# Kernel tuning notes

Measured on AMD Instinct MI355X. Metric: run time of the kernel, lower is better.

Reference implementation:

```python
import jax, jax.numpy as jnp
import numpy as np

V = 100000
E = 1600000
IN_CH = 128
HEADS = 4
OUT_CH = 16
NEG_SLOPE = 0.2


def setup_inputs() -> dict:
    key = jax.random.key(0)
    k1, k2, k3, k4, k5 = jax.random.split(key, 5)
    x = jax.random.normal(k1, (V, IN_CH), dtype=jnp.float32)
    edge_index = jax.random.randint(k2, (2, E), 0, V, dtype=jnp.int32)
    # Xavier-ish scaled params
    W = jax.random.normal(k3, (IN_CH, HEADS * OUT_CH), dtype=jnp.float32) / np.sqrt(IN_CH)
    a_src = jax.random.normal(k4, (HEADS, OUT_CH), dtype=jnp.float32) / np.sqrt(OUT_CH)
    a_dst = jax.random.normal(k5, (HEADS, OUT_CH), dtype=jnp.float32) / np.sqrt(OUT_CH)
    return {"x": x, "edge_index": edge_index, "W": W, "a_src": a_src, "a_dst": a_dst}


def reference(x, edge_index, W, a_src, a_dst):
    v = x.shape[0]
    h, cout = a_src.shape
    z = (x @ W).reshape(v, h, cout)                      # [V,H,C]
    src, dst = edge_index[0], edge_index[1]
    # per-node attention logits, then gather at edges (same math as gather-then-dot)
    e_src = jnp.einsum("vhc,hc->vh", z, a_src)           # [V,H]
    e_dst = jnp.einsum("vhc,hc->vh", z, a_dst)           # [V,H]
    e = jax.nn.leaky_relu(e_src[src] + e_dst[dst], NEG_SLOPE)  # [E,H]
    # scatter softmax over dst per head
    m = jax.ops.segment_max(e, dst, num_segments=v)      # [V,H]
    # nodes with no incoming edges get -inf max; edges never reference them
    exp_e = jnp.exp(e - m[dst])                          # [E,H]
    denom = jax.ops.segment_sum(exp_e, dst, num_segments=v)  # [V,H]
    alpha = exp_e / (denom[dst] + 1e-9)                  # [E,H]
    # scatter aggregation of weighted source features
    agg = jax.ops.segment_sum(z[src] * alpha[:, :, None], dst, num_segments=v)  # [V,H,C]
    out = jax.nn.elu(agg)
    return out.reshape(v, h * cout)
```

## Files before the change

kernel.cpp:

```cpp
#include <hip/hip_runtime.h>
#include <hip/hip_bf16.h>
#include <cstdint>

#define NV 100000
#define NE 1600000
#define KIN 128
#define NH 4
#define NC 16
#define NF 64
#define NBKT 1563
#define BCAP 1216
#define EPW 16
#define BINWG 391
#define GEMMWG 1563
#define XSTR 136

typedef __attribute__((ext_vector_type(8))) short bf16x8;
typedef __attribute__((ext_vector_type(4))) float f32x4;

__device__ __forceinline__ short f2bf(float f) {
    unsigned u = __float_as_uint(f);
    return (short)((u + 0x7FFFu + ((u >> 16) & 1u)) >> 16);
}

__device__ __forceinline__ unsigned enc11(float w) {
    unsigned t = (__float_as_uint(w) + 0x10000u) >> 17;
    t = min(max(t, 7168u), 9215u);
    return t - 7168u;
}

__global__ __launch_bounds__(256) void k_prep(
    const float* __restrict__ W, const float* __restrict__ a_src,
    const float* __restrict__ a_dst, short* __restrict__ wfrag,
    int* __restrict__ gcur)
{
    const int g = blockIdx.x * 256 + threadIdx.x;
    if (g < NBKT) gcur[g] = 0;
    if (g < 1280) {
        const int lane = g & 63;
        const int ctks = g >> 6;
        const int ct = ctks >> 2, ks = ctks & 3;
        const int n = lane & 15, quad = lane >> 4;
        short* dst = wfrag + (size_t)g * 8;
#pragma unroll
        for (int j = 0; j < 8; ++j) {
            const int k = ks * 32 + quad * 8 + j;
            float v = 0.f;
            if (ct < 4) {
                v = W[k * NF + ct * 16 + n];
            } else if (n < 8) {
                const int h = n & 3;
                const float* __restrict__ a =
                    (n < 4) ? (a_src + h * 16) : (a_dst + h * 16);
                for (int c = 0; c < 16; ++c)
                    v += W[k * NF + h * 16 + c] * a[c];
            }
            dst[j] = f2bf(v);
        }
    }
}

__global__ __launch_bounds__(256) void k_front(
    const float* __restrict__ x, const short* __restrict__ wfrag,
    __hip_bfloat16* __restrict__ z, float* __restrict__ esrc,
    float* __restrict__ edst,
    const int* __restrict__ ei, int* __restrict__ gcur,
    unsigned* __restrict__ barr)
{
    __shared__ union SM {
        struct { int hist[NBKT]; int base[NBKT]; } bin;
        short xs[64 * XSTR];
    } sm;

    if (blockIdx.x % 5 == 0) {
        int* hist = sm.bin.hist;
        int* base = sm.bin.base;
        const int t = threadIdx.x;
        const int e0 = (blockIdx.x / 5) * (256 * EPW);

        for (int i = t; i < NBKT; i += 256) hist[i] = 0;
        __syncthreads();

        unsigned pk[EPW];
        short bk[EPW];
#pragma unroll
        for (int i = 0; i < EPW; ++i) {
            const int e = e0 + i * 256 + t;
            if (e < NE) {
                const int s = ei[e];
                const int d = ei[NE + e];
                const int bkt = d >> 6;
                bk[i] = (short)bkt;
                pk[i] = ((unsigned)(d & 63) << 17) | (unsigned)s;
                atomicAdd(&hist[bkt], 1);
            } else {
                bk[i] = -1;
            }
        }
        __syncthreads();
        for (int i = t; i < NBKT; i += 256) {
            const int c = hist[i];
            base[i] = c ? atomicAdd(&gcur[i], c) : 0;
            hist[i] = 0;
        }
        __syncthreads();
#pragma unroll
        for (int i = 0; i < EPW; ++i) {
            if (bk[i] >= 0) {
                const int bkt = bk[i];
                const int pos = base[bkt] + atomicAdd(&hist[bkt], 1);
                if (pos < BCAP)
                    barr[(size_t)bkt * BCAP + pos] = pk[i];
            }
        }
    } else {
        short* xs = sm.xs;
        const int t = threadIdx.x;
        const int bb = blockIdx.x - blockIdx.x / 5 - 1;
        const float4* __restrict__ x4 = (const float4*)x;

#pragma unroll
        for (int i = 0; i < 8; ++i) {
            const int li = i * 256 + t;
            const int idx = bb * 2048 + li;
            float4 v = make_float4(0.f, 0.f, 0.f, 0.f);
            if (idx < NV * (KIN / 4)) v = x4[idx];
            const unsigned lo = (unsigned)(unsigned short)f2bf(v.x)
                              | ((unsigned)(unsigned short)f2bf(v.y) << 16);
            const unsigned hi = (unsigned)(unsigned short)f2bf(v.z)
                              | ((unsigned)(unsigned short)f2bf(v.w) << 16);
            *(uint2*)&xs[(li >> 5) * XSTR + (li & 31) * 4] = make_uint2(lo, hi);
        }
        __syncthreads();

        const int wv = t >> 6;
        const int lane = t & 63;
        const int n = lane & 15;
        const int quad = lane >> 4;

        bf16x8 bf[20];
        const bf16x8* __restrict__ wf = (const bf16x8*)wfrag;
#pragma unroll
        for (int i = 0; i < 20; ++i) bf[i] = wf[i * 64 + lane];

        const short* __restrict__ arow = &xs[(wv * 16 + n) * XSTR];
        f32x4 acc[5];
#pragma unroll
        for (int ct = 0; ct < 5; ++ct) acc[ct] = (f32x4){0.f, 0.f, 0.f, 0.f};

#pragma unroll
        for (int ks = 0; ks < 4; ++ks) {
            const bf16x8 af = *(const bf16x8*)(arow + ks * 32 + quad * 8);
#pragma unroll
            for (int ct = 0; ct < 5; ++ct)
                acc[ct] = __builtin_amdgcn_mfma_f32_16x16x32_bf16(
                    af, bf[ct * 4 + ks], acc[ct], 0, 0, 0);
        }

        unsigned short* __restrict__ zz = (unsigned short*)z;
#pragma unroll
        for (int ct = 0; ct < 4; ++ct) {
#pragma unroll
            for (int reg = 0; reg < 4; ++reg) {
                const int r_g = bb * 64 + wv * 16 + quad * 4 + reg;
                if (r_g < NV)
                    zz[(size_t)r_g * NF + ct * 16 + n] =
                        (unsigned short)f2bf(acc[ct][reg]);
            }
        }
#pragma unroll
        for (int reg = 0; reg < 4; ++reg) {
            const int r_g = bb * 64 + wv * 16 + quad * 4 + reg;
            if (r_g < NV && n < 8) {
                const float v = acc[4][reg];
                if (n < 4) esrc[r_g * NH + n] = v;
                else       edst[r_g * NH + (n - 4)] = v;
            }
        }
    }
}

__global__ __launch_bounds__(256) void k_back(
    const int* __restrict__ gcur, const unsigned* __restrict__ barr,
    const float* __restrict__ esrc, const float* __restrict__ edst,
    const __hip_bfloat16* __restrict__ z, float* __restrict__ out)
{
    __shared__ __align__(16) unsigned arr[BCAP];
    __shared__ unsigned long long rec[BCAP];
    __shared__ int hist[64], off[64], cur[64];
    __shared__ float4 led[64];
    const int t = threadIdx.x;
    const int b = blockIdx.x;
    int f = gcur[b]; if (f > BCAP) f = BCAP;
    const unsigned* __restrict__ bp = barr + (size_t)b * BCAP;

    if (t < 64) {
        hist[t] = 0;
        cur[t] = 0;
        const int d = b * 64 + t;
        led[t] = (d < NV) ? *(const float4*)(edst + (size_t)d * 4)
                          : make_float4(0.f, 0.f, 0.f, 0.f);
    }
    __syncthreads();
    const int f4 = f >> 2;
    for (int i = t; i < f4; i += 256) {
        const uint4 v = ((const uint4*)bp)[i];
        ((uint4*)arr)[i] = v;
        atomicAdd(&hist[v.x >> 17], 1);
        atomicAdd(&hist[v.y >> 17], 1);
        atomicAdd(&hist[v.z >> 17], 1);
        atomicAdd(&hist[v.w >> 17], 1);
    }
    for (int i = (f4 << 2) + t; i < f; i += 256) {
        const unsigned v = bp[i];
        arr[i] = v;
        atomicAdd(&hist[v >> 17], 1);
    }
    __syncthreads();
    if (t < 64) off[t] = hist[t];
    __syncthreads();
    for (int s = 1; s < 64; s <<= 1) {
        const int v = (t < 64 && t >= s) ? off[t - s] : 0;
        __syncthreads();
        if (t < 64) off[t] += v;
        __syncthreads();
    }
    if (t < 64) off[t] -= hist[t];
    __syncthreads();

    for (int i = t; i < f; i += 256) {
        const unsigned p = arr[i];
        const int dl = p >> 17;
        const unsigned s = p & 0x1FFFFu;
        const int slot = off[dl] + atomicAdd(&cur[dl], 1);
        const float4 e4 = *(const float4*)(esrc + (size_t)s * 4);
        const float4 ed = led[dl];
        float ev;
        ev = e4.x + ed.x; ev = ev > 0.f ? ev : 0.2f * ev;
        const unsigned w0 = enc11(__expf(ev));
        ev = e4.y + ed.y; ev = ev > 0.f ? ev : 0.2f * ev;
        const unsigned w1 = enc11(__expf(ev));
        ev = e4.z + ed.z; ev = ev > 0.f ? ev : 0.2f * ev;
        const unsigned w2 = enc11(__expf(ev));
        ev = e4.w + ed.w; ev = ev > 0.f ? ev : 0.2f * ev;
        const unsigned w3 = enc11(__expf(ev));
        rec[slot] = (unsigned long long)s
            | ((unsigned long long)w0 << 17)
            | ((unsigned long long)w1 << 28)
            | ((unsigned long long)w2 << 39)
            | ((unsigned long long)w3 << 50);
    }
    __syncthreads();

    const int wv = t >> 6;
    const int lane = t & 63;
    const int quad = lane >> 4;
    const int li = lane & 15;
    const int sh = 17 + 11 * (li >> 2);
    const unsigned short* __restrict__ zb = (const unsigned short*)z + li * 4;

    for (int k = 0; k < 16; ++k) {
        const int dl = (k << 2) | wv;
        const int d = b * 64 + dl;
        const int begin = off[dl];
        const int nd = hist[dl];
        float a0 = 0.f, a1 = 0.f, a2 = 0.f, a3 = 0.f, den = 0.f;
        for (int j = 0; j < nd; j += 8) {
            const int je0 = j + quad;
            const int je1 = je0 + 4;
            const unsigned long long r0 = (je0 < nd) ? rec[begin + je0] : 0ull;
            const unsigned long long r1 = (je1 < nd) ? rec[begin + je1] : 0ull;
            const unsigned s0 = (unsigned)r0 & 0x1FFFFu;
            const unsigned s1 = (unsigned)r1 & 0x1FFFFu;
            const float w0 = __uint_as_float(
                ((((unsigned)(r0 >> sh)) & 0x7FFu) + 7168u) << 17);
            const float w1 = __uint_as_float(
                ((((unsigned)(r1 >> sh)) & 0x7FFu) + 7168u) << 17);
            const uint2 zv0 = *(const uint2*)(zb + ((size_t)s0 << 6));
            const uint2 zv1 = *(const uint2*)(zb + ((size_t)s1 << 6));
            a0 = fmaf(w0, __uint_as_float(zv0.x << 16), a0);
            a1 = fmaf(w0, __uint_as_float(zv0.x & 0xFFFF0000u), a1);
            a2 = fmaf(w0, __uint_as_float(zv0.y << 16), a2);
            a3 = fmaf(w0, __uint_as_float(zv0.y & 0xFFFF0000u), a3);
            den += w0;
            a0 = fmaf(w1, __uint_as_float(zv1.x << 16), a0);
            a1 = fmaf(w1, __uint_as_float(zv1.x & 0xFFFF0000u), a1);
            a2 = fmaf(w1, __uint_as_float(zv1.y << 16), a2);
            a3 = fmaf(w1, __uint_as_float(zv1.y & 0xFFFF0000u), a3);
            den += w1;
        }
        a0 += __shfl_xor(a0, 16); a0 += __shfl_xor(a0, 32);
        a1 += __shfl_xor(a1, 16); a1 += __shfl_xor(a1, 32);
        a2 += __shfl_xor(a2, 16); a2 += __shfl_xor(a2, 32);
        a3 += __shfl_xor(a3, 16); a3 += __shfl_xor(a3, 32);
        den += __shfl_xor(den, 16); den += __shfl_xor(den, 32);
        if (lane < 16 && d < NV) {
            const float id = 1.f / (den + 1e-9f);
            float v0 = a0 * id, v1 = a1 * id, v2 = a2 * id, v3 = a3 * id;
            v0 = v0 > 0.f ? v0 : __expf(v0) - 1.f;
            v1 = v1 > 0.f ? v1 : __expf(v1) - 1.f;
            v2 = v2 > 0.f ? v2 : __expf(v2) - 1.f;
            v3 = v3 > 0.f ? v3 : __expf(v3) - 1.f;
            *(float4*)(out + (size_t)d * NF + li * 4) =
                make_float4(v0, v1, v2, v3);
        }
    }
}

extern "C" void kernel_launch(void* const* d_in, const int* in_sizes, int n_in,
                              void* d_out, int out_size, void* d_ws, size_t ws_size,
                              hipStream_t stream)
{
    const float* x     = (const float*)d_in[0];
    const int*   ei    = (const int*)d_in[1];
    const float* W     = (const float*)d_in[2];
    const float* a_src = (const float*)d_in[3];
    const float* a_dst = (const float*)d_in[4];
    float* out = (float*)d_out;

    char* p = (char*)d_ws;
    __hip_bfloat16* z = (__hip_bfloat16*)p;  p += (size_t)NV * NF * 2;
    float* esrc = (float*)p;                 p += (size_t)NV * NH * 4;
    float* edst = (float*)p;                 p += (size_t)NV * NH * 4;
    int*   gcur = (int*)p;                   p += (size_t)NBKT * 4;
    p = (char*)(((uintptr_t)p + 255) & ~(uintptr_t)255);
    short* wfrag = (short*)p;                p += (size_t)1280 * 8 * 2;
    p = (char*)(((uintptr_t)p + 255) & ~(uintptr_t)255);
    unsigned* barr = (unsigned*)p;           p += (size_t)NBKT * BCAP * 4;

    k_prep<<<7, 256, 0, stream>>>(W, a_src, a_dst, wfrag, gcur);
    k_front<<<BINWG + GEMMWG, 256, 0, stream>>>(x, wfrag, z, esrc, edst,
                                                ei, gcur, barr);
    k_back<<<NBKT, 256, 0, stream>>>(gcur, barr, esrc, edst, z, out);
}
```

Measured before the change: 179.2 us.

## Fuse prep, front, and back kernels into one cooperative persistent kernel

Merges the three kernel launches into a single cooperative kernel that runs a persistent grid sized from occupancy. Grid-wide syncs now separate the weight-prep, bin/GEMM, and aggregation phases, and blocks loop over work items. This removes two kernel launch gaps and the tail drain between phases. In exchange the grid is capped at occupancy times 256 CUs, the shared-memory union is larger (which may lower occupancy), and the grid syncs add their own cost.

```diff
diff --git a/kernel.cpp b/kernel.cpp
--- a/kernel.cpp
+++ b/kernel.cpp
@@ -1,6 +1,9 @@
 #include <hip/hip_runtime.h>
 #include <hip/hip_bf16.h>
+#include <hip/hip_cooperative_groups.h>
 #include <cstdint>
+
+namespace cg = cooperative_groups;
 
 #define NV 100000
 #define NE 1600000
@@ -13,6 +16,7 @@
 #define EPW 16
 #define BINWG 391
 #define GEMMWG 1563
+#define NITEMS 1954
 #define XSTR 136
 
 typedef __attribute__((ext_vector_type(8))) short bf16x8;
@@ -29,14 +33,35 @@
     return t - 7168u;
 }
 
-__global__ __launch_bounds__(256) void k_prep(
+__global__ __launch_bounds__(256) void k_fused(
+    const float* __restrict__ x, const int* __restrict__ ei,
     const float* __restrict__ W, const float* __restrict__ a_src,
-    const float* __restrict__ a_dst, short* __restrict__ wfrag,
-    int* __restrict__ gcur)
+    const float* __restrict__ a_dst,
+    __hip_bfloat16* __restrict__ z, float* __restrict__ esrc,
+    float* __restrict__ edst, int* __restrict__ gcur,
+    short* __restrict__ wfrag, unsigned* __restrict__ barr,
+    float* __restrict__ out)
 {
-    const int g = blockIdx.x * 256 + threadIdx.x;
-    if (g < NBKT) gcur[g] = 0;
-    if (g < 1280) {
+    __shared__ __align__(16) union SM {
+        struct { int hist[NBKT]; int base[NBKT]; } bin;
+        short xs[64 * XSTR];
+        struct {
+            unsigned arr[BCAP];
+            unsigned long long rec[BCAP];
+            int hist[64], off[64], cur[64];
+            float4 led[64];
+        } back;
+    } sm;
+
+    cg::grid_group grid = cg::this_grid();
+    const int t = threadIdx.x;
+    const int bid = blockIdx.x;
+    const int gsz = gridDim.x;
+    const int gtid = bid * 256 + t;
+    const int gth = gsz * 256;
+
+    for (int i = gtid; i < NBKT; i += gth) gcur[i] = 0;
+    for (int g = gtid; g < 1280; g += gth) {
         const int lane = g & 63;
         const int ctks = g >> 6;
         const int ct = ctks >> 2, ks = ctks & 3;
@@ -58,251 +83,237 @@
             dst[j] = f2bf(v);
         }
     }
-}
-
-__global__ __launch_bounds__(256) void k_front(
-    const float* __restrict__ x, const short* __restrict__ wfrag,
-    __hip_bfloat16* __restrict__ z, float* __restrict__ esrc,
-    float* __restrict__ edst,
-    const int* __restrict__ ei, int* __restrict__ gcur,
-    unsigned* __restrict__ barr)
-{
-    __shared__ union SM {
-        struct { int hist[NBKT]; int base[NBKT]; } bin;
-        short xs[64 * XSTR];
-    } sm;
-
-    if (blockIdx.x % 5 == 0) {
-        int* hist = sm.bin.hist;
-        int* base = sm.bin.base;
-        const int t = threadIdx.x;
-        const int e0 = (blockIdx.x / 5) * (256 * EPW);
-
-        for (int i = t; i < NBKT; i += 256) hist[i] = 0;
-        __syncthreads();
-
-        unsigned pk[EPW];
-        short bk[EPW];
-#pragma unroll
-        for (int i = 0; i < EPW; ++i) {
-            const int e = e0 + i * 256 + t;
-            if (e < NE) {
-                const int s = ei[e];
-                const int d = ei[NE + e];
-                const int bkt = d >> 6;
-                bk[i] = (short)bkt;
-                pk[i] = ((unsigned)(d & 63) << 17) | (unsigned)s;
-                atomicAdd(&hist[bkt], 1);
-            } else {
-                bk[i] = -1;
-            }
-        }
-        __syncthreads();
-        for (int i = t; i < NBKT; i += 256) {
-            const int c = hist[i];
-            base[i] = c ? atomicAdd(&gcur[i], c) : 0;
-            hist[i] = 0;
-        }
-        __syncthreads();
-#pragma unroll
-        for (int i = 0; i < EPW; ++i) {
-            if (bk[i] >= 0) {
-                const int bkt = bk[i];
-                const int pos = base[bkt] + atomicAdd(&hist[bkt], 1);
-                if (pos < BCAP)
-                    barr[(size_t)bkt * BCAP + pos] = pk[i];
-            }
-        }
-    } else {
-        short* xs = sm.xs;
-        const int t = threadIdx.x;
-        const int bb = blockIdx.x - blockIdx.x / 5 - 1;
-        const float4* __restrict__ x4 = (const float4*)x;
-
-#pragma unroll
-        for (int i = 0; i < 8; ++i) {
-            const int li = i * 256 + t;
-            const int idx = bb * 2048 + li;
-            float4 v = make_float4(0.f, 0.f, 0.f, 0.f);
-            if (idx < NV * (KIN / 4)) v = x4[idx];
-            const unsigned lo = (unsigned)(unsigned short)f2bf(v.x)
-                              | ((unsigned)(unsigned short)f2bf(v.y) << 16);
-            const unsigned hi = (unsigned)(unsigned short)f2bf(v.z)
-                              | ((unsigned)(unsigned short)f2bf(v.w) << 16);
-            *(uint2*)&xs[(li >> 5) * XSTR + (li & 31) * 4] = make_uint2(lo, hi);
+    __threadfence();
+    grid.sync();
+
+    for (int it = bid; it < NITEMS; it += gsz) {
+        __syncthreads();
+        if (it % 5 == 0) {
+            int* hist = sm.bin.hist;
+            int* base = sm.bin.base;
+            const int e0 = (it / 5) * (256 * EPW);
+
+            for (int i = t; i < NBKT; i += 256) hist[i] = 0;
+            __syncthreads();
+
+            unsigned pk[EPW];
+            short bk[EPW];
+#pragma unroll
+            for (int i = 0; i < EPW; ++i) {
+                const int e = e0 + i * 256 + t;
+                if (e < NE) {
+                    const int s = ei[e];
+                    const int d = ei[NE + e];
+                    const int bkt = d >> 6;
+                    bk[i] = (short)bkt;
+                    pk[i] = ((unsigned)(d & 63) << 17) | (unsigned)s;
+                    atomicAdd(&hist[bkt], 1);
+                } else {
+                    bk[i] = -1;
+                }
+            }
+            __syncthreads();
+            for (int i = t; i < NBKT; i += 256) {
+                const int c = hist[i];
+                base[i] = c ? atomicAdd(&gcur[i], c) : 0;
+                hist[i] = 0;
+            }
+            __syncthreads();
+#pragma unroll
+            for (int i = 0; i < EPW; ++i) {
+                if (bk[i] >= 0) {
+                    const int bkt = bk[i];
+                    const int pos = base[bkt] + atomicAdd(&hist[bkt], 1);
+                    if (pos < BCAP)
+                        barr[(size_t)bkt * BCAP + pos] = pk[i];
+                }
+            }
+        } else {
+            short* xs = sm.xs;
+            const int idg = it - it / 5 - 1;
+            const float4* __restrict__ x4 = (const float4*)x;
+
+#pragma unroll
+            for (int i = 0; i < 8; ++i) {
+                const int li = i * 256 + t;
+                const int idx = idg * 2048 + li;
+                float4 v = make_float4(0.f, 0.f, 0.f, 0.f);
+                if (idx < NV * (KIN / 4)) v = x4[idx];
+                const unsigned lo = (unsigned)(unsigned short)f2bf(v.x)
+                                  | ((unsigned)(unsigned short)f2bf(v.y) << 16);
+                const unsigned hi = (unsigned)(unsigned short)f2bf(v.z)
+                                  | ((unsigned)(unsigned short)f2bf(v.w) << 16);
+                *(uint2*)&xs[(li >> 5) * XSTR + (li & 31) * 4] =
+                    make_uint2(lo, hi);
+            }
+            __syncthreads();
+
+            const int wv = t >> 6;
+            const int lane = t & 63;
+            const int n = lane & 15;
+            const int quad = lane >> 4;
+
+            bf16x8 bf[20];
+            const bf16x8* __restrict__ wf = (const bf16x8*)wfrag;
+#pragma unroll
+            for (int i = 0; i < 20; ++i) bf[i] = wf[i * 64 + lane];
+
+            const short* __restrict__ arow = &xs[(wv * 16 + n) * XSTR];
+            f32x4 acc[5];
+#pragma unroll
+            for (int ct = 0; ct < 5; ++ct) acc[ct] = (f32x4){0.f, 0.f, 0.f, 0.f};
+
+#pragma unroll
+            for (int ks = 0; ks < 4; ++ks) {
+                const bf16x8 af = *(const bf16x8*)(arow + ks * 32 + quad * 8);
+#pragma unroll
+                for (int ct = 0; ct < 5; ++ct)
+                    acc[ct] = __builtin_amdgcn_mfma_f32_16x16x32_bf16(
+                        af, bf[ct * 4 + ks], acc[ct], 0, 0, 0);
+            }
+
+            unsigned short* __restrict__ zz = (unsigned short*)z;
+#pragma unroll
+            for (int ct = 0; ct < 4; ++ct) {
+#pragma unroll
+                for (int reg = 0; reg < 4; ++reg) {
+                    const int r_g = idg * 64 + wv * 16 + quad * 4 + reg;
+                    if (r_g < NV)
+                        zz[(size_t)r_g * NF + ct * 16 + n] =
+                            (unsigned short)f2bf(acc[ct][reg]);
+                }
+            }
+#pragma unroll
+            for (int reg = 0; reg < 4; ++reg) {
+                const int r_g = idg * 64 + wv * 16 + quad * 4 + reg;
+                if (r_g < NV && n < 8) {
+                    const float v = acc[4][reg];
+                    if (n < 4) esrc[r_g * NH + n] = v;
+                    else       edst[r_g * NH + (n - 4)] = v;
+                }
+            }
+        }
+    }
+    __threadfence();
+    grid.sync();
+
+    for (int b = bid; b < NBKT; b += gsz) {
+        __syncthreads();
+        auto& B = sm.back;
+        int f = gcur[b]; if (f > BCAP) f = BCAP;
+        const unsigned* __restrict__ bp = barr + (size_t)b * BCAP;
+
+        if (t < 64) {
+            B.hist[t] = 0;
+            B.cur[t] = 0;
+            const int d = b * 64 + t;
+            B.led[t] = (d < NV) ? *(const float4*)(edst + (size_t)d * 4)
+                                : make_float4(0.f, 0.f, 0.f, 0.f);
+        }
+        __syncthreads();
+        const int f4 = f >> 2;
+        for (int i = t; i < f4; i += 256) {
+            const uint4 v = ((const uint4*)bp)[i];
+            ((uint4*)B.arr)[i] = v;
+            atomicAdd(&B.hist[v.x >> 17], 1);
+            atomicAdd(&B.hist[v.y >> 17], 1);
+            atomicAdd(&B.hist[v.z >> 17], 1);
+            atomicAdd(&B.hist[v.w >> 17], 1);
+        }
+        for (int i = (f4 << 2) + t; i < f; i += 256) {
+            const unsigned v = bp[i];
+            B.arr[i] = v;
+            atomicAdd(&B.hist[v >> 17], 1);
+        }
+        __syncthreads();
+        if (t < 64) B.off[t] = B.hist[t];
+        __syncthreads();
+        for (int s = 1; s < 64; s <<= 1) {
+            const int v = (t < 64 && t >= s) ? B.off[t - s] : 0;
+            __syncthreads();
+            if (t < 64) B.off[t] += v;
+            __syncthreads();
+        }
+        if (t < 64) B.off[t] -= B.hist[t];
+        __syncthreads();
+
+        for (int i = t; i < f; i += 256) {
+            const unsigned p = B.arr[i];
+            const int dl = p >> 17;
+            const unsigned s = p & 0x1FFFFu;
+            const int slot = B.off[dl] + atomicAdd(&B.cur[dl], 1);
+            const float4 e4 = *(const float4*)(esrc + (size_t)s * 4);
+            const float4 ed = B.led[dl];
+            float ev;
+            ev = e4.x + ed.x; ev = ev > 0.f ? ev : 0.2f * ev;
+            const unsigned w0 = enc11(__expf(ev));
+            ev = e4.y + ed.y; ev = ev > 0.f ? ev : 0.2f * ev;
+            const unsigned w1 = enc11(__expf(ev));
+            ev = e4.z + ed.z; ev = ev > 0.f ? ev : 0.2f * ev;
+            const unsigned w2 = enc11(__expf(ev));
+            ev = e4.w + ed.w; ev = ev > 0.f ? ev : 0.2f * ev;
+            const unsigned w3 = enc11(__expf(ev));
+            B.rec[slot] = (unsigned long long)s
+                | ((unsigned long long)w0 << 17)
+                | ((unsigned long long)w1 << 28)
+                | ((unsigned long long)w2 << 39)
+                | ((unsigned long long)w3 << 50);
         }
         __syncthreads();
 
         const int wv = t >> 6;
         const int lane = t & 63;
-        const int n = lane & 15;
         const int quad = lane >> 4;
-
-        bf16x8 bf[20];
-        const bf16x8* __restrict__ wf = (const bf16x8*)wfrag;
-#pragma unroll
-        for (int i = 0; i < 20; ++i) bf[i] = wf[i * 64 + lane];
-
-        const short* __restrict__ arow = &xs[(wv * 16 + n) * XSTR];
-        f32x4 acc[5];
-#pragma unroll
-        for (int ct = 0; ct < 5; ++ct) acc[ct] = (f32x4){0.f, 0.f, 0.f, 0.f};
-
-#pragma unroll
-        for (int ks = 0; ks < 4; ++ks) {
-            const bf16x8 af = *(const bf16x8*)(arow + ks * 32 + quad * 8);
-#pragma unroll
-            for (int ct = 0; ct < 5; ++ct)
-                acc[ct] = __builtin_amdgcn_mfma_f32_16x16x32_bf16(
-                    af, bf[ct * 4 + ks], acc[ct], 0, 0, 0);
-        }
-
-        unsigned short* __restrict__ zz = (unsigned short*)z;
-#pragma unroll
-        for (int ct = 0; ct < 4; ++ct) {
-#pragma unroll
-            for (int reg = 0; reg < 4; ++reg) {
-                const int r_g = bb * 64 + wv * 16 + quad * 4 + reg;
-                if (r_g < NV)
-                    zz[(size_t)r_g * NF + ct * 16 + n] =
-                        (unsigned short)f2bf(acc[ct][reg]);
-            }
-        }
-#pragma unroll
-        for (int reg = 0; reg < 4; ++reg) {
-            const int r_g = bb * 64 + wv * 16 + quad * 4 + reg;
-            if (r_g < NV && n < 8) {
-                const float v = acc[4][reg];
-                if (n < 4) esrc[r_g * NH + n] = v;
-                else       edst[r_g * NH + (n - 4)] = v;
-            }
-        }
-    }
-}
-
-__global__ __launch_bounds__(256) void k_back(
-    const int* __restrict__ gcur, const unsigned* __restrict__ barr,
-    const float* __restrict__ esrc, const float* __restrict__ edst,
-    const __hip_bfloat16* __restrict__ z, float* __restrict__ out)
-{
-    __shared__ __align__(16) unsigned arr[BCAP];
-    __shared__ unsigned long long rec[BCAP];
-    __shared__ int hist[64], off[64], cur[64];
-    __shared__ float4 led[64];
-    const int t = threadIdx.x;
-    const int b = blockIdx.x;
-    int f = gcur[b]; if (f > BCAP) f = BCAP;
-    const unsigned* __restrict__ bp = barr + (size_t)b * BCAP;
-
-    if (t < 64) {
-        hist[t] = 0;
-        cur[t] = 0;
-        const int d = b * 64 + t;
-        led[t] = (d < NV) ? *(const float4*)(edst + (size_t)d * 4)
-                          : make_float4(0.f, 0.f, 0.f, 0.f);
-    }
-    __syncthreads();
-    const int f4 = f >> 2;
-    for (int i = t; i < f4; i += 256) {
-        const uint4 v = ((const uint4*)bp)[i];
-        ((uint4*)arr)[i] = v;
-        atomicAdd(&hist[v.x >> 17], 1);
-        atomicAdd(&hist[v.y >> 17], 1);
-        atomicAdd(&hist[v.z >> 17], 1);
-        atomicAdd(&hist[v.w >> 17], 1);
-    }
-    for (int i = (f4 << 2) + t; i < f; i += 256) {
-        const unsigned v = bp[i];
-        arr[i] = v;
-        atomicAdd(&hist[v >> 17], 1);
-    }
-    __syncthreads();
-    if (t < 64) off[t] = hist[t];
-    __syncthreads();
-    for (int s = 1; s < 64; s <<= 1) {
-        const int v = (t < 64 && t >= s) ? off[t - s] : 0;
-        __syncthreads();
-        if (t < 64) off[t] += v;
-        __syncthreads();
-    }
-    if (t < 64) off[t] -= hist[t];
-    __syncthreads();
-
-    for (int i = t; i < f; i += 256) {
-        const unsigned p = arr[i];
-        const int dl = p >> 17;
-        const unsigned s = p & 0x1FFFFu;
-        const int slot = off[dl] + atomicAdd(&cur[dl], 1);
-        const float4 e4 = *(const float4*)(esrc + (size_t)s * 4);
-        const float4 ed = led[dl];
-        float ev;
-        ev = e4.x + ed.x; ev = ev > 0.f ? ev : 0.2f * ev;
-        const unsigned w0 = enc11(__expf(ev));
-        ev = e4.y + ed.y; ev = ev > 0.f ? ev : 0.2f * ev;
-        const unsigned w1 = enc11(__expf(ev));
-        ev = e4.z + ed.z; ev = ev > 0.f ? ev : 0.2f * ev;
-        const unsigned w2 = enc11(__expf(ev));
-        ev = e4.w + ed.w; ev = ev > 0.f ? ev : 0.2f * ev;
-        const unsigned w3 = enc11(__expf(ev));
-        rec[slot] = (unsigned long long)s
-            | ((unsigned long long)w0 << 17)
-            | ((unsigned long long)w1 << 28)
-            | ((unsigned long long)w2 << 39)
-            | ((unsigned long long)w3 << 50);
-    }
-    __syncthreads();
-
-    const int wv = t >> 6;
-    const int lane = t & 63;
-    const int quad = lane >> 4;
-    const int li = lane & 15;
-    const int sh = 17 + 11 * (li >> 2);
-    const unsigned short* __restrict__ zb = (const unsigned short*)z + li * 4;
-
-    for (int k = 0; k < 16; ++k) {
-        const int dl = (k << 2) | wv;
-        const int d = b * 64 + dl;
-        const int begin = off[dl];
-        const int nd = hist[dl];
-        float a0 = 0.f, a1 = 0.f, a2 = 0.f, a3 = 0.f, den = 0.f;
-        for (int j = 0; j < nd; j += 8) {
-            const int je0 = j + quad;
-            const int je1 = je0 + 4;
-            const unsigned long long r0 = (je0 < nd) ? rec[begin + je0] : 0ull;
-            const unsigned long long r1 = (je1 < nd) ? rec[begin + je1] : 0ull;
-            const unsigned s0 = (unsigned)r0 & 0x1FFFFu;
-            const unsigned s1 = (unsigned)r1 & 0x1FFFFu;
-            const float w0 = __uint_as_float(
-                ((((unsigned)(r0 >> sh)) & 0x7FFu) + 7168u) << 17);
-            const float w1 = __uint_as_float(
-                ((((unsigned)(r1 >> sh)) & 0x7FFu) + 7168u) << 17);
-            const uint2 zv0 = *(const uint2*)(zb + ((size_t)s0 << 6));
-            const uint2 zv1 = *(const uint2*)(zb + ((size_t)s1 << 6));
-            a0 = fmaf(w0, __uint_as_float(zv0.x << 16), a0);
-            a1 = fmaf(w0, __uint_as_float(zv0.x & 0xFFFF0000u), a1);
-            a2 = fmaf(w0, __uint_as_float(zv0.y << 16), a2);
-            a3 = fmaf(w0, __uint_as_float(zv0.y & 0xFFFF0000u), a3);
-            den += w0;
-            a0 = fmaf(w1, __uint_as_float(zv1.x << 16), a0);
-            a1 = fmaf(w1, __uint_as_float(zv1.x & 0xFFFF0000u), a1);
-            a2 = fmaf(w1, __uint_as_float(zv1.y << 16), a2);
-            a3 = fmaf(w1, __uint_as_float(zv1.y & 0xFFFF0000u), a3);
-            den += w1;
-        }
-        a0 += __shfl_xor(a0, 16); a0 += __shfl_xor(a0, 32);
-        a1 += __shfl_xor(a1, 16); a1 += __shfl_xor(a1, 32);
-        a2 += __shfl_xor(a2, 16); a2 += __shfl_xor(a2, 32);
-        a3 += __shfl_xor(a3, 16); a3 += __shfl_xor(a3, 32);
-        den += __shfl_xor(den, 16); den += __shfl_xor(den, 32);
-        if (lane < 16 && d < NV) {
-            const float id = 1.f / (den + 1e-9f);
-            float v0 = a0 * id, v1 = a1 * id, v2 = a2 * id, v3 = a3 * id;
-            v0 = v0 > 0.f ? v0 : __expf(v0) - 1.f;
-            v1 = v1 > 0.f ? v1 : __expf(v1) - 1.f;
-            v2 = v2 > 0.f ? v2 : __expf(v2) - 1.f;
-            v3 = v3 > 0.f ? v3 : __expf(v3) - 1.f;
-            *(float4*)(out + (size_t)d * NF + li * 4) =
-                make_float4(v0, v1, v2, v3);
+        const int li = lane & 15;
+        const int sh = 17 + 11 * (li >> 2);
+        const unsigned short* __restrict__ zb =
+            (const unsigned short*)z + li * 4;
+
+        for (int k = 0; k < 16; ++k) {
+            const int dl = (k << 2) | wv;
+            const int d = b * 64 + dl;
+            const int begin = B.off[dl];
+            const int nd = B.hist[dl];
+            float a0 = 0.f, a1 = 0.f, a2 = 0.f, a3 = 0.f, den = 0.f;
+            for (int j = 0; j < nd; j += 8) {
+                const int je0 = j + quad;
+                const int je1 = je0 + 4;
+                const unsigned long long r0 = (je0 < nd) ? B.rec[begin + je0] : 0ull;
+                const unsigned long long r1 = (je1 < nd) ? B.rec[begin + je1] : 0ull;
+                const unsigned s0 = (unsigned)r0 & 0x1FFFFu;
+                const unsigned s1 = (unsigned)r1 & 0x1FFFFu;
+                const float w0 = __uint_as_float(
+                    ((((unsigned)(r0 >> sh)) & 0x7FFu) + 7168u) << 17);
+                const float w1 = __uint_as_float(
+                    ((((unsigned)(r1 >> sh)) & 0x7FFu) + 7168u) << 17);
+                const uint2 zv0 = *(const uint2*)(zb + ((size_t)s0 << 6));
+                const uint2 zv1 = *(const uint2*)(zb + ((size_t)s1 << 6));
+                a0 = fmaf(w0, __uint_as_float(zv0.x << 16), a0);
+                a1 = fmaf(w0, __uint_as_float(zv0.x & 0xFFFF0000u), a1);
+                a2 = fmaf(w0, __uint_as_float(zv0.y << 16), a2);
+                a3 = fmaf(w0, __uint_as_float(zv0.y & 0xFFFF0000u), a3);
+                den += w0;
+                a0 = fmaf(w1, __uint_as_float(zv1.x << 16), a0);
+                a1 = fmaf(w1, __uint_as_float(zv1.x & 0xFFFF0000u), a1);
+                a2 = fmaf(w1, __uint_as_float(zv1.y << 16), a2);
+                a3 = fmaf(w1, __uint_as_float(zv1.y & 0xFFFF0000u), a3);
+                den += w1;
+            }
+            a0 += __shfl_xor(a0, 16); a0 += __shfl_xor(a0, 32);
+            a1 += __shfl_xor(a1, 16); a1 += __shfl_xor(a1, 32);
+            a2 += __shfl_xor(a2, 16); a2 += __shfl_xor(a2, 32);
+            a3 += __shfl_xor(a3, 16); a3 += __shfl_xor(a3, 32);
+            den += __shfl_xor(den, 16); den += __shfl_xor(den, 32);
+            if (lane < 16 && d < NV) {
+                const float id = 1.f / (den + 1e-9f);
+                float v0 = a0 * id, v1 = a1 * id, v2 = a2 * id, v3 = a3 * id;
+                v0 = v0 > 0.f ? v0 : __expf(v0) - 1.f;
+                v1 = v1 > 0.f ? v1 : __expf(v1) - 1.f;
+                v2 = v2 > 0.f ? v2 : __expf(v2) - 1.f;
+                v3 = v3 > 0.f ? v3 : __expf(v3) - 1.f;
+                *(float4*)(out + (size_t)d * NF + li * 4) =
+                    make_float4(v0, v1, v2, v3);
+            }
         }
     }
 }
@@ -328,8 +339,19 @@
     p = (char*)(((uintptr_t)p + 255) & ~(uintptr_t)255);
     unsigned* barr = (unsigned*)p;           p += (size_t)NBKT * BCAP * 4;
 
-    k_prep<<<7, 256, 0, stream>>>(W, a_src, a_dst, wfrag, gcur);
-    k_front<<<BINWG + GEMMWG, 256, 0, stream>>>(x, wfrag, z, esrc, edst,
-                                                ei, gcur, barr);
-    k_back<<<NBKT, 256, 0, stream>>>(gcur, barr, esrc, edst, z, out);
+    static int nb = -1;
+    if (nb < 0) {
+        if (hipOccupancyMaxActiveBlocksPerMultiprocessor(&nb, k_fused, 256, 0)
+                != hipSuccess || nb <= 0)
+            nb = 4;
+        if (nb > 8) nb = 8;
+    }
+    int gridn = nb * 256;
+    if (gridn > NITEMS) gridn = NITEMS;
+
+    void* args[] = { (void*)&x, (void*)&ei, (void*)&W, (void*)&a_src,
+                     (void*)&a_dst, (void*)&z, (void*)&esrc, (void*)&edst,
+                     (void*)&gcur, (void*)&wfrag, (void*)&barr, (void*)&out };
+    hipLaunchCooperativeKernel((const void*)k_fused, dim3(gridn), dim3(256),
+                               args, 0, stream);
 }
```

New measurement: 434.6 us. 143% more time.
